# Performance work log

Measured on AMD Instinct MI355X. Metric: run time of the kernel, lower is better.

## Reference

```python
import jax, jax.numpy as jnp
import numpy as np

DIM, K_NN, RADIUS, HIDDEN = 128, 4, 2.5, 64
B, T, N = 32, 64, 25


def setup_inputs() -> dict:
    key = jax.random.key(0)
    ks = jax.random.split(key, 12)
    s = 0.02
    return {
        "emb": jax.random.normal(ks[0], (B, T, N, DIM), jnp.float32),
        "bboxes": jax.random.uniform(ks[1], (B, T, N, 4), jnp.float32),
        "person_mask": jax.random.uniform(ks[2], (B, T, N)) < 0.9,
        "edge_w1": jax.random.normal(ks[3], (2 * DIM + 3, HIDDEN), jnp.float32) * s,
        "edge_b1": jnp.zeros((HIDDEN,), jnp.float32),
        "edge_w2": jax.random.normal(ks[4], (HIDDEN, DIM), jnp.float32) * s,
        "edge_b2": jnp.zeros((DIM,), jnp.float32),
        "node_w1": jax.random.normal(ks[5], (2 * DIM, HIDDEN), jnp.float32) * s,
        "node_b1": jnp.zeros((HIDDEN,), jnp.float32),
        "node_w2": jax.random.normal(ks[6], (HIDDEN, DIM), jnp.float32) * s,
        "node_b2": jnp.zeros((DIM,), jnp.float32),
        "ln_g": jnp.ones((DIM,), jnp.float32),
        "ln_b": jnp.zeros((DIM,), jnp.float32),
    }


def _forward(emb, bboxes, person_mask, edge_w1, edge_b1, edge_w2, edge_b2,
             node_w1, node_b1, node_w2, node_b2, ln_g, ln_b):
    b, t, n, d = emb.shape
    BT = b * t
    x = emb.reshape(BT, n, d)
    boxes = bboxes.reshape(BT, n, 4)
    mask = person_mask.reshape(BT, n)

    cx, cy = boxes[..., 0], boxes[..., 1]
    h = jnp.maximum(boxes[..., 3], 1e-6)
    dx = cx[:, :, None] - cx[:, None, :]            # [BT,N,N]
    dy = cy[:, :, None] - cy[:, None, :]
    dist = jnp.sqrt(dx * dx + dy * dy + 1e-6)
    scale = h[:, :, None]
    dx_n, dy_n, dist_n = dx / scale, dy / scale, dist / scale

    eye = jnp.eye(n, dtype=bool)[None]
    pair_valid = (mask[:, :, None] & mask[:, None, :]) & ~eye
    dist_for_knn = jnp.where(pair_valid, dist_n, 1e6)

    K = min(K_NN, max(n - 1, 1))
    neg_d, knn_idx = jax.lax.top_k(-dist_for_knn, K)  # smallest-K -> [BT,N,K]
    knn_dist = -neg_d

    nbr_valid = jnp.take_along_axis(pair_valid, knn_idx, axis=2)
    nbr_valid = nbr_valid & (knn_dist < RADIUS)

    # gather neighbor features: [BT,N,K,D]
    bt_idx = jnp.arange(BT)[:, None, None]
    x_j = x[bt_idx, knn_idx]
    x_i = jnp.broadcast_to(x[:, :, None, :], (BT, n, K, d))
    edge_all = jnp.stack([dx_n, dy_n, dist_n], axis=-1)  # [BT,N,N,3]
    e_ij = jnp.take_along_axis(edge_all, knn_idx[..., None], axis=2)  # [BT,N,K,3]

    msg_in = jnp.concatenate([x_i, x_j, e_ij], axis=-1)  # [BT,N,K,2D+3]
    msg = jax.nn.relu(msg_in @ edge_w1 + edge_b1) @ edge_w2 + edge_b2
    nbr_f = nbr_valid.astype(msg.dtype)
    msg = msg * nbr_f[..., None]
    denom = jnp.maximum(nbr_f.sum(axis=2, keepdims=True), 1.0)
    agg = msg.sum(axis=2) / denom                    # [BT,N,D]

    upd_in = jnp.concatenate([x, agg], axis=-1)
    delta = jax.nn.relu(upd_in @ node_w1 + node_b1) @ node_w2 + node_b2
    has_nbr = jnp.any(nbr_valid, axis=2, keepdims=True)
    delta = delta * has_nbr.astype(delta.dtype)

    y = x + delta
    mu = y.mean(axis=-1, keepdims=True)
    var = y.var(axis=-1, keepdims=True)
    y = (y - mu) * jax.lax.rsqrt(var + 1e-5) * ln_g + ln_b
    out = y * mask[..., None].astype(y.dtype)
    return out.reshape(b, t, n, d)


def reference(emb, bboxes, person_mask, edge_w1, edge_b1, edge_w2, edge_b2,
              node_w1, node_b1, node_w2, node_b2, ln_g, ln_b):
    return _forward(emb, bboxes, person_mask, edge_w1, edge_b1, edge_w2, edge_b2,
                    node_w1, node_b1, node_w2, node_b2, ln_g, ln_b)
```

## Files before the change

### kernel.cpp

```cpp
#include <hip/hip_runtime.h>

#define NN   25
#define DD   128
#define HH   64
#define KK   4
#define RADF 2.5f

#define XBP  136
#define HSP  72

#define O_W1T  0
#define O_W2NT 16896
#define O_N1LO 20992
#define O_N2T  29184
#define O_B2N  37376

typedef __attribute__((ext_vector_type(8))) short  short8;
typedef __attribute__((ext_vector_type(4))) float  f32x4;

__device__ __forceinline__ ushort f2bf(float x) {
    uint u = __float_as_uint(x);
    u += 0x7fffu + ((u >> 16) & 1u);
    return (ushort)(u >> 16);
}
__device__ __forceinline__ float bf2f(ushort u) {
    return __uint_as_float((uint)u << 16);
}
__device__ __forceinline__ uint pack2(float a, float b) {
    return (uint)f2bf(a) | ((uint)f2bf(b) << 16);
}
__device__ __forceinline__ short8 ldw(const ushort* p) {
    return *reinterpret_cast<const short8*>(p);
}
#define MFMA16(a, b, c) __builtin_amdgcn_mfma_f32_16x16x32_bf16((a), (b), (c), 0, 0, 0)

__global__ void prep_kernel(const float* __restrict__ ew1, const float* __restrict__ ew2,
                            const float* __restrict__ eb2, const float* __restrict__ nw1,
                            const float* __restrict__ nw2, ushort* __restrict__ w) {
    int tid = blockIdx.x * blockDim.x + threadIdx.x;
    int stride = gridDim.x * blockDim.x;
    for (int e = tid; e < 259 * 64; e += stride) {
        int k = e >> 6, c = e & 63;
        w[O_W1T + c * 264 + k] = f2bf(ew1[e]);
    }
    for (int e = tid; e < 64 * 128; e += stride) {
        int c = e >> 7, k = e & 127;
        w[O_N1LO + e] = f2bf(nw1[(size_t)k * 64 + c]);
    }
    for (int e = tid; e < 128 * 64; e += stride) {
        int d = e >> 6, k = e & 63;
        w[O_N2T + e] = f2bf(nw2[(size_t)k * 128 + d]);
    }
    for (int e = tid; e < 64 * 64; e += stride) {
        int c = e >> 6, k = e & 63;
        float acc = 0.f;
        for (int d = 0; d < DD; ++d)
            acc += ew2[(size_t)k * DD + d] * nw1[(size_t)(DD + d) * HH + c];
        w[O_W2NT + e] = f2bf(acc);
    }
    for (int c = tid; c < HH; c += stride) {
        float acc = 0.f;
        for (int d = 0; d < DD; ++d)
            acc += eb2[d] * nw1[(size_t)(DD + d) * HH + c];
        reinterpret_cast<float*>(w + O_B2N)[c] = acc;
    }
}

__global__ __launch_bounds__(128, 4) void ig12_kernel(
    const float* __restrict__ emb,
    const float* __restrict__ bboxes,
    const int*   __restrict__ pmask,
    const float* __restrict__ ew1f,
    const float* __restrict__ eb1,
    const float* __restrict__ nb1,
    const float* __restrict__ nb2,
    const float* __restrict__ lng,
    const float* __restrict__ lnb,
    const ushort* __restrict__ W,
    float* __restrict__ out)
{
    const int bt  = blockIdx.x;
    const int t   = threadIdx.x;
    const int wv  = t >> 6;
    const int ln  = t & 63;
    const int g   = ln >> 4;
    const int r16 = ln & 15;
    const int cb  = 2 * wv;
    const int cb4 = 4 * wv;

    __shared__ ushort s_xb[NN * XBP];
    __shared__ ushort s_hxi[NN * HSP];
    __shared__ ushort s_hs[NN * HSP];
    __shared__ ushort s_nxi[NN * HSP];
    __shared__ __align__(16) char s_misc[1600];
    __shared__ short  s_idxs[NN][KK];
    __shared__ float  s_meta[NN][4];

    float (*s_ev)[KK][4] = reinterpret_cast<float(*)[KK][4]>(s_misc);
    float (*s_red)[2][2] = reinterpret_cast<float(*)[2][2]>(s_misc);
    ushort* s_g1v = s_hxi;

    if (wv == 0) {
        const float4* src4 = reinterpret_cast<const float4*>(emb + (size_t)bt * (NN * DD));
        for (int u = ln; u < NN * 16; u += 64) {
            int row = u >> 4, q = u & 15;
            float4 f0 = src4[row * 32 + q * 2];
            float4 f1 = src4[row * 32 + q * 2 + 1];
            uint4 p;
            p.x = pack2(f0.x, f0.y); p.y = pack2(f0.z, f0.w);
            p.z = pack2(f1.x, f1.y); p.w = pack2(f1.z, f1.w);
            *reinterpret_cast<uint4*>(&s_xb[row * XBP + q * 8]) = p;
        }
    } else {
        const int n = (ln < NN) ? ln : NN - 1;
        const float4 b4 = *reinterpret_cast<const float4*>(bboxes + ((size_t)bt * NN + n) * 4);
        const float cxn = b4.x, cyn = b4.y;
        const float hvn = fmaxf(b4.w, 1e-6f);
        const int   mn  = pmask[(size_t)bt * NN + n];
        const float inv = 1.0f / hvn;
        float best[KK] = {1e30f, 1e30f, 1e30f, 1e30f};
        int   bidx[KK] = {0, 0, 0, 0};
        for (int j = 0; j < NN; ++j) {
            float cxj = __shfl(cxn, j);
            float cyj = __shfl(cyn, j);
            int   mj  = __shfl(mn, j);
            float dx = cxn - cxj, dy = cyn - cyj;
            float dn = sqrtf(fmaf(dx, dx, fmaf(dy, dy, 1e-6f))) * inv;
            bool  pv = (mn != 0) && (mj != 0) && (j != n);
            float cv = pv ? dn : 1e6f;
            int   ci = j;
#pragma unroll
            for (int kk = 0; kk < KK; ++kk) {
                if (cv < best[kk]) {
                    float tv = best[kk]; best[kk] = cv; cv = tv;
                    int   ti = bidx[kk]; bidx[kk] = ci; ci = ti;
                }
            }
        }
        float cnt = 0.f;
        float e0v[KK], e1v[KK], e2v[KK], vvv[KK];
#pragma unroll
        for (int k = 0; k < KK; ++k) {
            int bj = bidx[k];
            float cxb = __shfl(cxn, bj);
            float cyb = __shfl(cyn, bj);
            float val = (best[k] < RADF) ? 1.f : 0.f;
            cnt += val;
            float dx = cxn - cxb, dy = cyn - cyb;
            e0v[k] = dx * inv;
            e1v[k] = dy * inv;
            e2v[k] = sqrtf(fmaf(dx, dx, fmaf(dy, dy, 1e-6f))) * inv;
            vvv[k] = val;
        }
        if (ln < NN) {
#pragma unroll
            for (int k = 0; k < KK; ++k) {
                s_ev[n][k][0] = e0v[k];
                s_ev[n][k][1] = e1v[k];
                s_ev[n][k][2] = e2v[k];
                s_ev[n][k][3] = vvv[k];
                s_idxs[n][k]  = (short)bidx[k];
            }
            s_meta[n][0] = cnt;
            s_meta[n][1] = 1.0f / fmaxf(cnt, 1.0f);
            s_meta[n][2] = (cnt > 0.f) ? 1.f : 0.f;
            s_meta[n][3] = mn ? 1.f : 0.f;
        }
    }
    __syncthreads();

    {
        int na1 = 16 + r16; if (na1 > 24) na1 = 24;
        const ushort* A0 = s_xb + r16 * XBP + g * 8;
        const ushort* A1 = s_xb + na1 * XBP + g * 8;
        f32x4 ce[2][2] = {};
        f32x4 cn[2][2] = {};
#pragma unroll
        for (int kt = 0; kt < 4; ++kt) {
            short8 a0 = ldw(A0 + kt * 32);
            short8 a1 = ldw(A1 + kt * 32);
#pragma unroll
            for (int ntl = 0; ntl < 2; ++ntl) {
                short8 be = ldw(W + O_W1T  + (size_t)(16 * (cb + ntl) + r16) * 264 + kt * 32 + g * 8);
                short8 bn = ldw(W + O_N1LO + (size_t)(16 * (cb + ntl) + r16) * 128 + kt * 32 + g * 8);
                ce[0][ntl] = MFMA16(a0, be, ce[0][ntl]);
                ce[1][ntl] = MFMA16(a1, be, ce[1][ntl]);
                cn[0][ntl] = MFMA16(a0, bn, cn[0][ntl]);
                cn[1][ntl] = MFMA16(a1, bn, cn[1][ntl]);
            }
        }
#pragma unroll
        for (int mt = 0; mt < 2; ++mt)
#pragma unroll
            for (int q = 0; q < 4; ++q) {
                int nr = 16 * mt + 4 * g + q;
                if (nr < 25) {
#pragma unroll
                    for (int ntl = 0; ntl < 2; ++ntl) {
                        int col = 16 * (cb + ntl) + r16;
                        s_hxi[nr * HSP + col] = f2bf(ce[mt][ntl][q]);
                        s_nxi[nr * HSP + col] = f2bf(cn[mt][ntl][q]);
                    }
                }
            }
    }

    {
        int jn[7];
#pragma unroll
        for (int T = 0; T < 7; ++T) {
            int r = 16 * T + r16; if (r > 99) r = 99;
            jn[T] = s_idxs[r >> 2][r & 3];
        }
        f32x4 c[7][2] = {};
#pragma unroll
        for (int kt = 0; kt < 4; ++kt) {
            short8 b0 = ldw(W + O_W1T + (size_t)(16 * (cb + 0) + r16) * 264 + 128 + kt * 32 + g * 8);
            short8 b1 = ldw(W + O_W1T + (size_t)(16 * (cb + 1) + r16) * 264 + 128 + kt * 32 + g * 8);
#pragma unroll
            for (int T = 0; T < 7; ++T) {
                short8 a = ldw(s_xb + jn[T] * XBP + kt * 32 + g * 8);
                c[T][0] = MFMA16(a, b0, c[T][0]);
                c[T][1] = MFMA16(a, b1, c[T][1]);
            }
        }
        float we0[2], we1[2], we2[2], bb1[2];
#pragma unroll
        for (int ntl = 0; ntl < 2; ++ntl) {
            int col = 16 * (cb + ntl) + r16;
            we0[ntl] = ew1f[256 * 64 + col];
            we1[ntl] = ew1f[257 * 64 + col];
            we2[ntl] = ew1f[258 * 64 + col];
            bb1[ntl] = eb1[col];
        }
#pragma unroll
        for (int T = 0; T < 7; ++T) {
            const int n = 4 * T + g;
            if (n < 25) {
                float v0 = s_ev[n][0][3], v1 = s_ev[n][1][3];
                float v2 = s_ev[n][2][3], v3 = s_ev[n][3][3];
                float e0q[4], e1q[4], e2q[4];
#pragma unroll
                for (int q = 0; q < 4; ++q) {
                    e0q[q] = s_ev[n][q][0]; e1q[q] = s_ev[n][q][1]; e2q[q] = s_ev[n][q][2];
                }
#pragma unroll
                for (int ntl = 0; ntl < 2; ++ntl) {
                    int col = 16 * (cb + ntl) + r16;
                    float base = bb1[ntl] + bf2f(s_hxi[n * HSP + col]);
                    float p0 = c[T][ntl][0] + base + e0q[0] * we0[ntl] + e1q[0] * we1[ntl] + e2q[0] * we2[ntl];
                    float p1 = c[T][ntl][1] + base + e0q[1] * we0[ntl] + e1q[1] * we1[ntl] + e2q[1] * we2[ntl];
                    float p2 = c[T][ntl][2] + base + e0q[2] * we0[ntl] + e1q[2] * we1[ntl] + e2q[2] * we2[ntl];
                    float p3 = c[T][ntl][3] + base + e0q[3] * we0[ntl] + e1q[3] * we1[ntl] + e2q[3] * we2[ntl];
                    float hs = fmaf(v0, fmaxf(p0, 0.f),
                               fmaf(v1, fmaxf(p1, 0.f),
                               fmaf(v2, fmaxf(p2, 0.f),
                                    v3 * fmaxf(p3, 0.f))));
                    s_hs[n * HSP + col] = f2bf(hs);
                }
            }
        }
    }
    __syncthreads();

    {
        int na1 = 16 + r16; if (na1 > 24) na1 = 24;
        const ushort* A0 = s_hs + r16 * HSP + g * 8;
        const ushort* A1 = s_hs + na1 * HSP + g * 8;
        f32x4 c[2][2] = {};
#pragma unroll
        for (int kt = 0; kt < 2; ++kt) {
            short8 a0 = ldw(A0 + kt * 32);
            short8 a1 = ldw(A1 + kt * 32);
#pragma unroll
            for (int ntl = 0; ntl < 2; ++ntl) {
                short8 b = ldw(W + O_W2NT + (size_t)(16 * (cb + ntl) + r16) * 64 + kt * 32 + g * 8);
                c[0][ntl] = MFMA16(a0, b, c[0][ntl]);
                c[1][ntl] = MFMA16(a1, b, c[1][ntl]);
            }
        }
        const float* b2Np = reinterpret_cast<const float*>(W + O_B2N);
#pragma unroll
        for (int ntl = 0; ntl < 2; ++ntl) {
            int col = 16 * (cb + ntl) + r16;
            float b2n = b2Np[col];
            float b1c = nb1[col];
#pragma unroll
            for (int mt = 0; mt < 2; ++mt)
#pragma unroll
                for (int q = 0; q < 4; ++q) {
                    int nr = 16 * mt + 4 * g + q;
                    if (nr < 25) {
                        float v = bf2f(s_nxi[nr * HSP + col]) + b1c
                                + s_meta[nr][1] * fmaf(s_meta[nr][0], b2n, c[mt][ntl][q]);
                        s_g1v[nr * HSP + col] = f2bf(fmaxf(v, 0.f));
                    }
                }
        }
    }
    __syncthreads();

    {
        int na1 = 16 + r16; if (na1 > 24) na1 = 24;
        const ushort* A0 = s_g1v + r16 * HSP + g * 8;
        const ushort* A1 = s_g1v + na1 * HSP + g * 8;
        f32x4 c[2][4] = {};
#pragma unroll
        for (int kt = 0; kt < 2; ++kt) {
            short8 a0 = ldw(A0 + kt * 32);
            short8 a1 = ldw(A1 + kt * 32);
#pragma unroll
            for (int ntl = 0; ntl < 4; ++ntl) {
                short8 b = ldw(W + O_N2T + (size_t)(16 * (cb4 + ntl) + r16) * 64 + kt * 32 + g * 8);
                c[0][ntl] = MFMA16(a0, b, c[0][ntl]);
                c[1][ntl] = MFMA16(a1, b, c[1][ntl]);
            }
        }
        float nb2c[4], glc[4], blc[4];
#pragma unroll
        for (int ntl = 0; ntl < 4; ++ntl) {
            int col = 16 * (cb4 + ntl) + r16;
            nb2c[ntl] = nb2[col];
            glc[ntl]  = lng[col];
            blc[ntl]  = lnb[col];
        }
        float y[2][4][4];
#pragma unroll
        for (int mt = 0; mt < 2; ++mt) {
#pragma unroll
            for (int q = 0; q < 4; ++q) {
                int nr = 16 * mt + 4 * g + q;
                int nc = nr < 25 ? nr : 24;
                float has = s_meta[nc][2];
                float a = 0.f, b = 0.f;
#pragma unroll
                for (int ntl = 0; ntl < 4; ++ntl) {
                    int col = 16 * (cb4 + ntl) + r16;
                    float yv = fmaf(has, c[mt][ntl][q] + nb2c[ntl], bf2f(s_xb[nc * XBP + col]));
                    y[mt][ntl][q] = yv;
                    a += yv;
                    b = fmaf(yv, yv, b);
                }
#pragma unroll
                for (int o = 1; o < 16; o <<= 1) {
                    a += __shfl_xor(a, o);
                    b += __shfl_xor(b, o);
                }
                if (r16 == 0 && nr < 25) {
                    s_red[nr][wv][0] = a;
                    s_red[nr][wv][1] = b;
                }
            }
        }
        __syncthreads();
#pragma unroll
        for (int mt = 0; mt < 2; ++mt) {
#pragma unroll
            for (int q = 0; q < 4; ++q) {
                int nr = 16 * mt + 4 * g + q;
                int nc = nr < 25 ? nr : 24;
                float S   = s_red[nc][0][0] + s_red[nc][1][0];
                float S2  = s_red[nc][0][1] + s_red[nc][1][1];
                float mu  = S * (1.0f / 128.0f);
                float var = S2 * (1.0f / 128.0f) - mu * mu;
                float rs  = rsqrtf(var + 1e-5f);
                float mk  = s_meta[nc][3];
                if (nr < 25) {
                    float* op = out + (size_t)bt * (NN * DD) + nr * DD;
#pragma unroll
                    for (int ntl = 0; ntl < 4; ++ntl) {
                        int col = 16 * (cb4 + ntl) + r16;
                        op[col] = fmaf((y[mt][ntl][q] - mu) * rs, glc[ntl], blc[ntl]) * mk;
                    }
                }
            }
        }
    }
}

extern "C" void kernel_launch(void* const* d_in, const int* in_sizes, int n_in,
                              void* d_out, int out_size, void* d_ws, size_t ws_size,
                              hipStream_t stream) {
    const float* emb    = (const float*)d_in[0];
    const float* bboxes = (const float*)d_in[1];
    const int*   pmask  = (const int*)  d_in[2];
    const float* ew1    = (const float*)d_in[3];
    const float* eb1    = (const float*)d_in[4];
    const float* ew2    = (const float*)d_in[5];
    const float* eb2    = (const float*)d_in[6];
    const float* nw1    = (const float*)d_in[7];
    const float* nb1    = (const float*)d_in[8];
    const float* nw2    = (const float*)d_in[9];
    const float* nb2    = (const float*)d_in[10];
    const float* lng    = (const float*)d_in[11];
    const float* lnb    = (const float*)d_in[12];
    float* out = (float*)d_out;
    ushort* W  = (ushort*)d_ws;

    prep_kernel<<<64, 256, 0, stream>>>(ew1, ew2, eb2, nw1, nw2, W);

    const int BT = in_sizes[2] / NN;
    ig12_kernel<<<BT, 128, 0, stream>>>(
        emb, bboxes, pmask, ew1, eb1, nb1, nb2, lng, lnb, W, out);
}
```

Baseline: 42.73 us.

## Split nodes across waves by row instead of columns to drop block barriers

Each of the two wavefronts now owns a disjoint set of nodes (13 and 12 rows) and computes all output columns for them, instead of splitting hidden and output columns between waves. This removes the inter-stage __syncthreads and the cross-wave LayerNorm reduction through shared memory, since each wave's row data stays wave-local. The emb load now uses both waves, and both waves compute kNN redundantly. The trade-off is fewer padded M-tiles but more weight-fragment loads per wave (all N columns), plus duplicated kNN work.

```diff
diff --git a/kernel.cpp b/kernel.cpp
--- a/kernel.cpp
+++ b/kernel.cpp
@@ -66,7 +66,7 @@
     }
 }
 
-__global__ __launch_bounds__(128, 4) void ig12_kernel(
+__global__ __launch_bounds__(128, 4) void ig17_kernel(
     const float* __restrict__ emb,
     const float* __restrict__ bboxes,
     const int*   __restrict__ pmask,
@@ -85,24 +85,25 @@
     const int ln  = t & 63;
     const int g   = ln >> 4;
     const int r16 = ln & 15;
-    const int cb  = 2 * wv;
-    const int cb4 = 4 * wv;
+
+    const int NB = wv ? 13 : 0;
+    const int NM = wv ? 12 : 13;
+    const int nT = wv ? 3 : 4;
+    const int ME = NM * KK;
 
     __shared__ ushort s_xb[NN * XBP];
     __shared__ ushort s_hxi[NN * HSP];
     __shared__ ushort s_hs[NN * HSP];
     __shared__ ushort s_nxi[NN * HSP];
-    __shared__ __align__(16) char s_misc[1600];
+    __shared__ float  s_ev[NN][KK][4];
     __shared__ short  s_idxs[NN][KK];
     __shared__ float  s_meta[NN][4];
 
-    float (*s_ev)[KK][4] = reinterpret_cast<float(*)[KK][4]>(s_misc);
-    float (*s_red)[2][2] = reinterpret_cast<float(*)[2][2]>(s_misc);
     ushort* s_g1v = s_hxi;
 
-    if (wv == 0) {
+    {
         const float4* src4 = reinterpret_cast<const float4*>(emb + (size_t)bt * (NN * DD));
-        for (int u = ln; u < NN * 16; u += 64) {
+        for (int u = t; u < NN * 16; u += 128) {
             int row = u >> 4, q = u & 15;
             float4 f0 = src4[row * 32 + q * 2];
             float4 f1 = src4[row * 32 + q * 2 + 1];
@@ -111,7 +112,8 @@
             p.z = pack2(f1.x, f1.y); p.w = pack2(f1.z, f1.w);
             *reinterpret_cast<uint4*>(&s_xb[row * XBP + q * 8]) = p;
         }
-    } else {
+    }
+    {
         const int n = (ln < NN) ? ln : NN - 1;
         const float4 b4 = *reinterpret_cast<const float4*>(bboxes + ((size_t)bt * NN + n) * 4);
         const float cxn = b4.x, cyn = b4.y;
@@ -152,7 +154,7 @@
             e2v[k] = sqrtf(fmaf(dx, dx, fmaf(dy, dy, 1e-6f))) * inv;
             vvv[k] = val;
         }
-        if (ln < NN) {
+        if (ln >= NB && ln < NB + NM) {
 #pragma unroll
             for (int k = 0; k < KK; ++k) {
                 s_ev[n][k][0] = e0v[k];
@@ -170,208 +172,190 @@
     __syncthreads();
 
     {
-        int na1 = 16 + r16; if (na1 > 24) na1 = 24;
-        const ushort* A0 = s_xb + r16 * XBP + g * 8;
-        const ushort* A1 = s_xb + na1 * XBP + g * 8;
-        f32x4 ce[2][2] = {};
-        f32x4 cn[2][2] = {};
+        const int ra = NB + ((r16 < NM) ? r16 : NM - 1);
+        const ushort* A0 = s_xb + ra * XBP + g * 8;
+        f32x4 ce[4] = {};
+        f32x4 cn[4] = {};
 #pragma unroll
         for (int kt = 0; kt < 4; ++kt) {
             short8 a0 = ldw(A0 + kt * 32);
-            short8 a1 = ldw(A1 + kt * 32);
-#pragma unroll
-            for (int ntl = 0; ntl < 2; ++ntl) {
-                short8 be = ldw(W + O_W1T  + (size_t)(16 * (cb + ntl) + r16) * 264 + kt * 32 + g * 8);
-                short8 bn = ldw(W + O_N1LO + (size_t)(16 * (cb + ntl) + r16) * 128 + kt * 32 + g * 8);
-                ce[0][ntl] = MFMA16(a0, be, ce[0][ntl]);
-                ce[1][ntl] = MFMA16(a1, be, ce[1][ntl]);
-                cn[0][ntl] = MFMA16(a0, bn, cn[0][ntl]);
-                cn[1][ntl] = MFMA16(a1, bn, cn[1][ntl]);
-            }
-        }
-#pragma unroll
-        for (int mt = 0; mt < 2; ++mt)
-#pragma unroll
-            for (int q = 0; q < 4; ++q) {
-                int nr = 16 * mt + 4 * g + q;
-                if (nr < 25) {
-#pragma unroll
-                    for (int ntl = 0; ntl < 2; ++ntl) {
-                        int col = 16 * (cb + ntl) + r16;
-                        s_hxi[nr * HSP + col] = f2bf(ce[mt][ntl][q]);
-                        s_nxi[nr * HSP + col] = f2bf(cn[mt][ntl][q]);
-                    }
-                }
-            }
-    }
-
-    {
-        int jn[7];
-#pragma unroll
-        for (int T = 0; T < 7; ++T) {
-            int r = 16 * T + r16; if (r > 99) r = 99;
-            jn[T] = s_idxs[r >> 2][r & 3];
-        }
-        f32x4 c[7][2] = {};
+#pragma unroll
+            for (int ntl = 0; ntl < 4; ++ntl) {
+                short8 be = ldw(W + O_W1T  + (size_t)(16 * ntl + r16) * 264 + kt * 32 + g * 8);
+                short8 bn = ldw(W + O_N1LO + (size_t)(16 * ntl + r16) * 128 + kt * 32 + g * 8);
+                ce[ntl] = MFMA16(a0, be, ce[ntl]);
+                cn[ntl] = MFMA16(a0, bn, cn[ntl]);
+            }
+        }
+#pragma unroll
+        for (int q = 0; q < 4; ++q) {
+            int nl = 4 * g + q;
+            if (nl < NM) {
+                int nr = NB + nl;
+#pragma unroll
+                for (int ntl = 0; ntl < 4; ++ntl) {
+                    int col = 16 * ntl + r16;
+                    s_hxi[nr * HSP + col] = f2bf(ce[ntl][q]);
+                    s_nxi[nr * HSP + col] = f2bf(cn[ntl][q]);
+                }
+            }
+        }
+    }
+
+#pragma unroll
+    for (int pass = 0; pass < 2; ++pass) {
+        const int T0 = 2 * pass;
+        const int tc = (nT - T0 > 2) ? 2 : (nT - T0);
+        int jn[2];
+#pragma unroll
+        for (int i = 0; i < 2; ++i) {
+            if (i < tc) {
+                int lr = 16 * (T0 + i) + r16; if (lr > ME - 1) lr = ME - 1;
+                jn[i] = s_idxs[NB + (lr >> 2)][lr & 3];
+            } else jn[i] = 0;
+        }
+        f32x4 c[2][4] = {};
 #pragma unroll
         for (int kt = 0; kt < 4; ++kt) {
-            short8 b0 = ldw(W + O_W1T + (size_t)(16 * (cb + 0) + r16) * 264 + 128 + kt * 32 + g * 8);
-            short8 b1 = ldw(W + O_W1T + (size_t)(16 * (cb + 1) + r16) * 264 + 128 + kt * 32 + g * 8);
-#pragma unroll
-            for (int T = 0; T < 7; ++T) {
-                short8 a = ldw(s_xb + jn[T] * XBP + kt * 32 + g * 8);
-                c[T][0] = MFMA16(a, b0, c[T][0]);
-                c[T][1] = MFMA16(a, b1, c[T][1]);
-            }
-        }
-        float we0[2], we1[2], we2[2], bb1[2];
-#pragma unroll
-        for (int ntl = 0; ntl < 2; ++ntl) {
-            int col = 16 * (cb + ntl) + r16;
+            short8 b[4];
+#pragma unroll
+            for (int ntl = 0; ntl < 4; ++ntl)
+                b[ntl] = ldw(W + O_W1T + (size_t)(16 * ntl + r16) * 264 + 128 + kt * 32 + g * 8);
+#pragma unroll
+            for (int i = 0; i < 2; ++i) {
+                if (i < tc) {
+                    short8 a = ldw(s_xb + jn[i] * XBP + kt * 32 + g * 8);
+#pragma unroll
+                    for (int ntl = 0; ntl < 4; ++ntl)
+                        c[i][ntl] = MFMA16(a, b[ntl], c[i][ntl]);
+                }
+            }
+        }
+        float we0[4], we1[4], we2[4], bb1[4];
+#pragma unroll
+        for (int ntl = 0; ntl < 4; ++ntl) {
+            int col = 16 * ntl + r16;
             we0[ntl] = ew1f[256 * 64 + col];
             we1[ntl] = ew1f[257 * 64 + col];
             we2[ntl] = ew1f[258 * 64 + col];
             bb1[ntl] = eb1[col];
         }
 #pragma unroll
-        for (int T = 0; T < 7; ++T) {
-            const int n = 4 * T + g;
-            if (n < 25) {
-                float v0 = s_ev[n][0][3], v1 = s_ev[n][1][3];
-                float v2 = s_ev[n][2][3], v3 = s_ev[n][3][3];
-                float e0q[4], e1q[4], e2q[4];
-#pragma unroll
-                for (int q = 0; q < 4; ++q) {
-                    e0q[q] = s_ev[n][q][0]; e1q[q] = s_ev[n][q][1]; e2q[q] = s_ev[n][q][2];
-                }
-#pragma unroll
-                for (int ntl = 0; ntl < 2; ++ntl) {
-                    int col = 16 * (cb + ntl) + r16;
-                    float base = bb1[ntl] + bf2f(s_hxi[n * HSP + col]);
-                    float p0 = c[T][ntl][0] + base + e0q[0] * we0[ntl] + e1q[0] * we1[ntl] + e2q[0] * we2[ntl];
-                    float p1 = c[T][ntl][1] + base + e0q[1] * we0[ntl] + e1q[1] * we1[ntl] + e2q[1] * we2[ntl];
-                    float p2 = c[T][ntl][2] + base + e0q[2] * we0[ntl] + e1q[2] * we1[ntl] + e2q[2] * we2[ntl];
-                    float p3 = c[T][ntl][3] + base + e0q[3] * we0[ntl] + e1q[3] * we1[ntl] + e2q[3] * we2[ntl];
-                    float hs = fmaf(v0, fmaxf(p0, 0.f),
-                               fmaf(v1, fmaxf(p1, 0.f),
-                               fmaf(v2, fmaxf(p2, 0.f),
-                                    v3 * fmaxf(p3, 0.f))));
-                    s_hs[n * HSP + col] = f2bf(hs);
-                }
-            }
-        }
-    }
-    __syncthreads();
-
-    {
-        int na1 = 16 + r16; if (na1 > 24) na1 = 24;
-        const ushort* A0 = s_hs + r16 * HSP + g * 8;
-        const ushort* A1 = s_hs + na1 * HSP + g * 8;
-        f32x4 c[2][2] = {};
+        for (int i = 0; i < 2; ++i) {
+            if (i < tc) {
+                const int nl = 4 * (T0 + i) + g;
+                if (nl < NM) {
+                    const int n = NB + nl;
+                    float v0 = s_ev[n][0][3], v1 = s_ev[n][1][3];
+                    float v2 = s_ev[n][2][3], v3 = s_ev[n][3][3];
+                    float e0q[4], e1q[4], e2q[4];
+#pragma unroll
+                    for (int q = 0; q < 4; ++q) {
+                        e0q[q] = s_ev[n][q][0]; e1q[q] = s_ev[n][q][1]; e2q[q] = s_ev[n][q][2];
+                    }
+#pragma unroll
+                    for (int ntl = 0; ntl < 4; ++ntl) {
+                        int col = 16 * ntl + r16;
+                        float base = bb1[ntl] + bf2f(s_hxi[n * HSP + col]);
+                        float p0 = c[i][ntl][0] + base + e0q[0] * we0[ntl] + e1q[0] * we1[ntl] + e2q[0] * we2[ntl];
+                        float p1 = c[i][ntl][1] + base + e0q[1] * we0[ntl] + e1q[1] * we1[ntl] + e2q[1] * we2[ntl];
+                        float p2 = c[i][ntl][2] + base + e0q[2] * we0[ntl] + e1q[2] * we1[ntl] + e2q[2] * we2[ntl];
+                        float p3 = c[i][ntl][3] + base + e0q[3] * we0[ntl] + e1q[3] * we1[ntl] + e2q[3] * we2[ntl];
+                        float hs = fmaf(v0, fmaxf(p0, 0.f),
+                                   fmaf(v1, fmaxf(p1, 0.f),
+                                   fmaf(v2, fmaxf(p2, 0.f),
+                                        v3 * fmaxf(p3, 0.f))));
+                        s_hs[n * HSP + col] = f2bf(hs);
+                    }
+                }
+            }
+        }
+    }
+
+    {
+        const int ra = NB + ((r16 < NM) ? r16 : NM - 1);
+        const ushort* A0 = s_hs + ra * HSP + g * 8;
+        f32x4 c[4] = {};
 #pragma unroll
         for (int kt = 0; kt < 2; ++kt) {
             short8 a0 = ldw(A0 + kt * 32);
-            short8 a1 = ldw(A1 + kt * 32);
-#pragma unroll
-            for (int ntl = 0; ntl < 2; ++ntl) {
-                short8 b = ldw(W + O_W2NT + (size_t)(16 * (cb + ntl) + r16) * 64 + kt * 32 + g * 8);
-                c[0][ntl] = MFMA16(a0, b, c[0][ntl]);
-                c[1][ntl] = MFMA16(a1, b, c[1][ntl]);
+#pragma unroll
+            for (int ntl = 0; ntl < 4; ++ntl) {
+                short8 b = ldw(W + O_W2NT + (size_t)(16 * ntl + r16) * 64 + kt * 32 + g * 8);
+                c[ntl] = MFMA16(a0, b, c[ntl]);
             }
         }
         const float* b2Np = reinterpret_cast<const float*>(W + O_B2N);
 #pragma unroll
-        for (int ntl = 0; ntl < 2; ++ntl) {
-            int col = 16 * (cb + ntl) + r16;
+        for (int ntl = 0; ntl < 4; ++ntl) {
+            int col = 16 * ntl + r16;
             float b2n = b2Np[col];
             float b1c = nb1[col];
 #pragma unroll
-            for (int mt = 0; mt < 2; ++mt)
-#pragma unroll
-                for (int q = 0; q < 4; ++q) {
-                    int nr = 16 * mt + 4 * g + q;
-                    if (nr < 25) {
-                        float v = bf2f(s_nxi[nr * HSP + col]) + b1c
-                                + s_meta[nr][1] * fmaf(s_meta[nr][0], b2n, c[mt][ntl][q]);
-                        s_g1v[nr * HSP + col] = f2bf(fmaxf(v, 0.f));
-                    }
-                }
-        }
-    }
-    __syncthreads();
-
-    {
-        int na1 = 16 + r16; if (na1 > 24) na1 = 24;
-        const ushort* A0 = s_g1v + r16 * HSP + g * 8;
-        const ushort* A1 = s_g1v + na1 * HSP + g * 8;
-        f32x4 c[2][4] = {};
+            for (int q = 0; q < 4; ++q) {
+                int nl = 4 * g + q;
+                if (nl < NM) {
+                    int nr = NB + nl;
+                    float v = bf2f(s_nxi[nr * HSP + col]) + b1c
+                            + s_meta[nr][1] * fmaf(s_meta[nr][0], b2n, c[ntl][q]);
+                    s_g1v[nr * HSP + col] = f2bf(fmaxf(v, 0.f));
+                }
+            }
+        }
+    }
+
+    {
+        const int ra = NB + ((r16 < NM) ? r16 : NM - 1);
+        const ushort* A0 = s_g1v + ra * HSP + g * 8;
+        f32x4 c[8] = {};
 #pragma unroll
         for (int kt = 0; kt < 2; ++kt) {
             short8 a0 = ldw(A0 + kt * 32);
-            short8 a1 = ldw(A1 + kt * 32);
-#pragma unroll
-            for (int ntl = 0; ntl < 4; ++ntl) {
-                short8 b = ldw(W + O_N2T + (size_t)(16 * (cb4 + ntl) + r16) * 64 + kt * 32 + g * 8);
-                c[0][ntl] = MFMA16(a0, b, c[0][ntl]);
-                c[1][ntl] = MFMA16(a1, b, c[1][ntl]);
-            }
-        }
-        float nb2c[4], glc[4], blc[4];
-#pragma unroll
-        for (int ntl = 0; ntl < 4; ++ntl) {
-            int col = 16 * (cb4 + ntl) + r16;
+#pragma unroll
+            for (int ntl = 0; ntl < 8; ++ntl) {
+                short8 b = ldw(W + O_N2T + (size_t)(16 * ntl + r16) * 64 + kt * 32 + g * 8);
+                c[ntl] = MFMA16(a0, b, c[ntl]);
+            }
+        }
+        float nb2c[8], glc[8], blc[8];
+#pragma unroll
+        for (int ntl = 0; ntl < 8; ++ntl) {
+            int col = 16 * ntl + r16;
             nb2c[ntl] = nb2[col];
             glc[ntl]  = lng[col];
             blc[ntl]  = lnb[col];
         }
-        float y[2][4][4];
-#pragma unroll
-        for (int mt = 0; mt < 2; ++mt) {
-#pragma unroll
-            for (int q = 0; q < 4; ++q) {
-                int nr = 16 * mt + 4 * g + q;
-                int nc = nr < 25 ? nr : 24;
-                float has = s_meta[nc][2];
-                float a = 0.f, b = 0.f;
-#pragma unroll
-                for (int ntl = 0; ntl < 4; ++ntl) {
-                    int col = 16 * (cb4 + ntl) + r16;
-                    float yv = fmaf(has, c[mt][ntl][q] + nb2c[ntl], bf2f(s_xb[nc * XBP + col]));
-                    y[mt][ntl][q] = yv;
-                    a += yv;
-                    b = fmaf(yv, yv, b);
-                }
-#pragma unroll
-                for (int o = 1; o < 16; o <<= 1) {
-                    a += __shfl_xor(a, o);
-                    b += __shfl_xor(b, o);
-                }
-                if (r16 == 0 && nr < 25) {
-                    s_red[nr][wv][0] = a;
-                    s_red[nr][wv][1] = b;
-                }
-            }
-        }
-        __syncthreads();
-#pragma unroll
-        for (int mt = 0; mt < 2; ++mt) {
-#pragma unroll
-            for (int q = 0; q < 4; ++q) {
-                int nr = 16 * mt + 4 * g + q;
-                int nc = nr < 25 ? nr : 24;
-                float S   = s_red[nc][0][0] + s_red[nc][1][0];
-                float S2  = s_red[nc][0][1] + s_red[nc][1][1];
-                float mu  = S * (1.0f / 128.0f);
-                float var = S2 * (1.0f / 128.0f) - mu * mu;
-                float rs  = rsqrtf(var + 1e-5f);
-                float mk  = s_meta[nc][3];
-                if (nr < 25) {
-                    float* op = out + (size_t)bt * (NN * DD) + nr * DD;
-#pragma unroll
-                    for (int ntl = 0; ntl < 4; ++ntl) {
-                        int col = 16 * (cb4 + ntl) + r16;
-                        op[col] = fmaf((y[mt][ntl][q] - mu) * rs, glc[ntl], blc[ntl]) * mk;
-                    }
+#pragma unroll
+        for (int q = 0; q < 4; ++q) {
+            int nl = 4 * g + q;
+            int ncl = (nl < NM) ? nl : NM - 1;
+            int nc  = NB + ncl;
+            float has = s_meta[nc][2];
+            float y[8];
+            float a = 0.f, b = 0.f;
+#pragma unroll
+            for (int ntl = 0; ntl < 8; ++ntl) {
+                int col = 16 * ntl + r16;
+                float yv = fmaf(has, c[ntl][q] + nb2c[ntl], bf2f(s_xb[nc * XBP + col]));
+                y[ntl] = yv;
+                a += yv;
+                b = fmaf(yv, yv, b);
+            }
+#pragma unroll
+            for (int o = 1; o < 16; o <<= 1) {
+                a += __shfl_xor(a, o);
+                b += __shfl_xor(b, o);
+            }
+            float mu  = a * (1.0f / 128.0f);
+            float var = b * (1.0f / 128.0f) - mu * mu;
+            float rs  = rsqrtf(var + 1e-5f);
+            float mk  = s_meta[nc][3];
+            if (nl < NM) {
+                float* op = out + (size_t)bt * (NN * DD) + nc * DD;
+#pragma unroll
+                for (int ntl = 0; ntl < 8; ++ntl) {
+                    int col = 16 * ntl + r16;
+                    op[col] = fmaf((y[ntl] - mu) * rs, glc[ntl], blc[ntl]) * mk;
                 }
             }
         }
@@ -400,6 +384,6 @@
     prep_kernel<<<64, 256, 0, stream>>>(ew1, ew2, eb2, nw1, nw2, W);
 
     const int BT = in_sizes[2] / NN;
-    ig12_kernel<<<BT, 128, 0, stream>>>(
+    ig17_kernel<<<BT, 128, 0, stream>>>(
         emb, bboxes, pmask, ew1, eb1, nb1, nb2, lng, lnb, W, out);
 }
```

Measured after the change: 58.36 us. 36.6% more time.
